# Optimization experiments

Hardware: AMD Instinct MI355X
Metric: run time of the kernel (lower is better)

Reference implementation:

```python
import jax, jax.numpy as jnp
import numpy as np

R, M, A = 512, 256, 256
B, L = 64, 4096


def setup_inputs() -> dict:
    key = jax.random.key(0)
    k1, k2, k3, k4, k5 = jax.random.split(key, 5)
    return {
        "hidden_state": jax.random.normal(k1, (B, R), dtype=jnp.float32),
        "feature_vectors": jax.random.normal(k2, (B, L, M), dtype=jnp.float32),
        "Wa": jax.random.normal(k3, (A, R), dtype=jnp.float32) / np.sqrt(R),
        "Ua": jax.random.normal(k4, (A, M), dtype=jnp.float32) / np.sqrt(M),
        "w": jax.random.normal(k5, (A, 1), dtype=jnp.float32),
        "ba": jnp.zeros((1, A), dtype=jnp.float32),
    }


def reference(hidden_state, feature_vectors, Wa, Ua, w, ba):
    # q: [B, A] broadcast over L; k: [B, L, A]
    q = hidden_state @ Wa.T + ba                      # [B, A]
    k = jnp.einsum("blm,am->bla", feature_vectors, Ua)  # [B, L, A]
    e = jnp.tanh(q[:, None, :] + k) @ w               # [B, L, 1]
    attn = jax.nn.softmax(e, axis=1)                  # softmax over L
    context = jnp.sum(attn * feature_vectors, axis=1)  # [B, M]
    return context
```

## Files before the change

### kernel.cpp

```cpp
#include <hip/hip_runtime.h>
#include <hip/hip_bf16.h>

#define B_  64
#define R_  512
#define M_  256
#define A_  256
#define L_  4096
#define TR_ 256
#define NT2_ (L_ / TR_)

typedef float    f32x4  __attribute__((ext_vector_type(4)));
typedef _Float16 f16x8  __attribute__((ext_vector_type(8)));
typedef _Float16 f16x4  __attribute__((ext_vector_type(4)));

__global__ __launch_bounds__(256) void k_prep(const float* __restrict__ Ua,
                                              _Float16* __restrict__ UaSw) {
  int gid = blockIdx.x * 256 + threadIdx.x;
  int a  = gid >> 6;
  int m0 = (gid & 63) * 4;
  f32x4 v = *(const f32x4*)(Ua + (size_t)a * M_ + m0);
  int t = a >> 4, l16 = a & 15;
  int s = m0 >> 5, quad = (m0 >> 3) & 3, j = m0 & 7;
  size_t idx = ((size_t)((t * 8 + s) * 64 + l16 * 4 + quad)) * 8 + j;
  f16x4 h;
  h[0] = (_Float16)v.x; h[1] = (_Float16)v.y;
  h[2] = (_Float16)v.z; h[3] = (_Float16)v.w;
  *(f16x4*)(UaSw + idx) = h;
}

__global__ __launch_bounds__(256) void k_q(const float* __restrict__ h,
                                           const float* __restrict__ Wa,
                                           const float* __restrict__ ba,
                                           float* __restrict__ q) {
  int b = blockIdx.x;
  int tid = threadIdx.x;
  int wv = tid >> 6, lane = tid & 63;
  const f32x4* hp = (const f32x4*)(h + (size_t)b * R_ + lane * 8);
  f32x4 h0 = hp[0], h1 = hp[1];
#pragma unroll 4
  for (int i = 0; i < 64; ++i) {
    int a = wv * 64 + i;
    const f32x4* wp = (const f32x4*)(Wa + (size_t)a * R_ + lane * 8);
    f32x4 w0 = wp[0], w1 = wp[1];
    f32x4 pr = h0 * w0 + h1 * w1;
    float p = (pr.x + pr.y) + (pr.z + pr.w);
#pragma unroll
    for (int m = 1; m < 64; m <<= 1) p += __shfl_xor(p, m);
    if (lane == 0) q[b * A_ + a] = p + ba[a];
  }
}

__global__ __launch_bounds__(256, 2) void k_main(const float* __restrict__ fv,
                                                 const _Float16* __restrict__ UaSw,
                                                 const float* __restrict__ q,
                                                 const float* __restrict__ w,
                                                 float* __restrict__ blkmax,
                                                 float* __restrict__ blksum,
                                                 float* __restrict__ blkacc) {
  __shared__ __align__(16) _Float16 sA[4][4096];
  __shared__ float sq[A_];
  __shared__ float sw[A_];
  __shared__ float sE[TR_];
  __shared__ float sRed[8];
  __shared__ float sAcc[4][M_];
  int tid = threadIdx.x;
  int b  = blockIdx.x >> 4;
  int l0 = (blockIdx.x & 15) * TR_;
  int wv = tid >> 6, lane = tid & 63;
  int quad = lane >> 4, l16 = lane & 15;

  sq[tid] = q[b * A_ + tid];
  sw[tid] = w[tid];

  int s_w  = lane >> 3;
  int qd_w = (lane >> 1) & 3;
  int jh_w = (lane & 1) * 4;
  _Float16* wbase = &sA[wv][0];

  f16x8 afrag[4][8];
#pragma unroll
  for (int c = 0; c < 4; ++c) {
    const float* rowp = fv + ((size_t)b * L_ + (size_t)(l0 + wv * 64 + c * 16)) * M_ + lane * 4;
#pragma unroll
    for (int i = 0; i < 16; ++i) {
      f32x4 v = *(const f32x4*)(rowp + (size_t)i * M_);
      f16x4 h;
      h[0] = (_Float16)v.x; h[1] = (_Float16)v.y;
      h[2] = (_Float16)v.z; h[3] = (_Float16)v.w;
      *(f16x4*)(wbase + s_w * 512 + (i * 4 + qd_w) * 8 + jh_w) = h;
    }
#pragma unroll
    for (int s = 0; s < 8; ++s)
      afrag[c][s] = *(const f16x8*)(wbase + s * 512 + (l16 * 4 + quad) * 8);
  }
  __syncthreads();

  float eacc[4][4] = {{0,0,0,0},{0,0,0,0},{0,0,0,0},{0,0,0,0}};

#pragma unroll 2
  for (int t = 0; t < 16; ++t) {
    f32x4 acc0 = 0.f, acc1 = 0.f, acc2 = 0.f, acc3 = 0.f;
    const f16x8* bp = (const f16x8*)(UaSw + ((size_t)(t * 8) * 64 + (l16 * 4 + quad)) * 8);
#pragma unroll
    for (int s = 0; s < 8; ++s) {
      f16x8 bf = bp[s * 64];
      acc0 = __builtin_amdgcn_mfma_f32_16x16x32_f16(afrag[0][s], bf, acc0, 0, 0, 0);
      acc1 = __builtin_amdgcn_mfma_f32_16x16x32_f16(afrag[1][s], bf, acc1, 0, 0, 0);
      acc2 = __builtin_amdgcn_mfma_f32_16x16x32_f16(afrag[2][s], bf, acc2, 0, 0, 0);
      acc3 = __builtin_amdgcn_mfma_f32_16x16x32_f16(afrag[3][s], bf, acc3, 0, 0, 0);
    }
    float qc = sq[t * 16 + l16], wc = sw[t * 16 + l16];
#pragma unroll
    for (int i = 0; i < 4; ++i) {
      float x0 = qc + acc0[i];
      eacc[0][i] += (1.0f - 2.0f * __builtin_amdgcn_rcpf(__expf(2.0f * x0) + 1.0f)) * wc;
      float x1 = qc + acc1[i];
      eacc[1][i] += (1.0f - 2.0f * __builtin_amdgcn_rcpf(__expf(2.0f * x1) + 1.0f)) * wc;
      float x2 = qc + acc2[i];
      eacc[2][i] += (1.0f - 2.0f * __builtin_amdgcn_rcpf(__expf(2.0f * x2) + 1.0f)) * wc;
      float x3 = qc + acc3[i];
      eacc[3][i] += (1.0f - 2.0f * __builtin_amdgcn_rcpf(__expf(2.0f * x3) + 1.0f)) * wc;
    }
  }

#pragma unroll
  for (int c = 0; c < 4; ++c)
#pragma unroll
    for (int i = 0; i < 4; ++i) {
      float v = eacc[c][i];
      v += __shfl_xor(v, 1); v += __shfl_xor(v, 2);
      v += __shfl_xor(v, 4); v += __shfl_xor(v, 8);
      if (l16 == 0) sE[wv * 64 + c * 16 + quad * 4 + i] = v;
    }
  __syncthreads();

  float m = sE[tid];
#pragma unroll
  for (int k = 1; k < 64; k <<= 1) m = fmaxf(m, __shfl_xor(m, k));
  if (lane == 0) sRed[wv] = m;
  __syncthreads();
  float mx = fmaxf(fmaxf(sRed[0], sRed[1]), fmaxf(sRed[2], sRed[3]));

  float p[4];
#pragma unroll
  for (int c = 0; c < 4; ++c) p[c] = __expf(sE[wv * 64 + c * 16 + l16] - mx);

  float ps = (quad == 0) ? ((p[0] + p[1]) + (p[2] + p[3])) : 0.f;
#pragma unroll
  for (int k = 1; k < 64; k <<= 1) ps += __shfl_xor(ps, k);
  if (lane == 0) sRed[4 + wv] = ps;

#pragma unroll
  for (int s = 0; s < 8; ++s) {
    float cj[8];
#pragma unroll
    for (int j = 0; j < 8; ++j)
      cj[j] = p[0] * (float)afrag[0][s][j] + p[1] * (float)afrag[1][s][j] +
              p[2] * (float)afrag[2][s][j] + p[3] * (float)afrag[3][s][j];
#pragma unroll
    for (int k = 1; k < 16; k <<= 1) {
#pragma unroll
      for (int j = 0; j < 8; ++j) cj[j] += __shfl_xor(cj[j], k);
    }
    if (l16 == 0) {
#pragma unroll
      for (int j = 0; j < 8; ++j) sAcc[wv][s * 32 + quad * 8 + j] = cj[j];
    }
  }
  __syncthreads();

  float colsum = (sAcc[0][tid] + sAcc[1][tid]) + (sAcc[2][tid] + sAcc[3][tid]);
  blkacc[(size_t)blockIdx.x * M_ + tid] = colsum;
  if (tid == 0) {
    blkmax[blockIdx.x] = mx;
    blksum[blockIdx.x] = (sRed[4] + sRed[5]) + (sRed[6] + sRed[7]);
  }
}

__global__ __launch_bounds__(256) void k_fin(const float* __restrict__ blkmax,
                                             const float* __restrict__ blksum,
                                             const float* __restrict__ blkacc,
                                             float* __restrict__ out) {
  __shared__ float sSc[NT2_];
  int b = blockIdx.x, t = threadIdx.x;
  float M = -1e30f;
#pragma unroll
  for (int i = 0; i < NT2_; ++i) M = fmaxf(M, blkmax[b * NT2_ + i]);
  if (t < NT2_) sSc[t] = __expf(blkmax[b * NT2_ + t] - M);
  __syncthreads();
  float acc = 0.f, S = 0.f;
#pragma unroll 4
  for (int i = 0; i < NT2_; ++i) {
    float sc = sSc[i];
    S += blksum[b * NT2_ + i] * sc;
    acc += blkacc[(size_t)(b * NT2_ + i) * M_ + t] * sc;
  }
  out[b * M_ + t] = acc / S;
}

extern "C" void kernel_launch(void* const* d_in, const int* in_sizes, int n_in,
                              void* d_out, int out_size, void* d_ws, size_t ws_size,
                              hipStream_t stream) {
  const float* h  = (const float*)d_in[0];
  const float* fv = (const float*)d_in[1];
  const float* Wa = (const float*)d_in[2];
  const float* Ua = (const float*)d_in[3];
  const float* w  = (const float*)d_in[4];
  const float* ba = (const float*)d_in[5];
  float* out = (float*)d_out;

  char* ws = (char*)d_ws;
  float*    q      = (float*)(ws);
  _Float16* UaSw   = (_Float16*)(ws + 65536);
  float*    blkmax = (float*)(ws + 196608);
  float*    blksum = (float*)(ws + 200704);
  float*    blkacc = (float*)(ws + 204800);

  k_prep<<<dim3(64), dim3(256), 0, stream>>>(Ua, UaSw);
  k_q<<<dim3(B_), dim3(256), 0, stream>>>(h, Wa, ba, q);
  k_main<<<dim3(B_ * NT2_), dim3(256), 0, stream>>>(fv, UaSw, q, w, blkmax, blksum, blkacc);
  k_fin<<<dim3(B_), dim3(256), 0, stream>>>(blkmax, blksum, blkacc, out);
}
```

Baseline: 466.1 us.

## Halve rows per block, raise occupancy, and software-prefetch Ua fragments

Each block now processes 128 sequence rows instead of 256, which doubles the grid to 2048 blocks and halves the per-thread A-fragment registers. Launch bounds are raised to 4 waves-per-EU. Ua B-fragments are prefetched one step ahead across the t/s loops. The finalize kernel and workspace offsets are resized for 32 partials per batch. The trade is that each Ua fragment load now feeds only two MFMAs instead of four, doubling total Ua traffic, and there are more partials to merge.

```diff
diff --git a/kernel.cpp b/kernel.cpp
--- a/kernel.cpp
+++ b/kernel.cpp
@@ -6,8 +6,8 @@
 #define M_  256
 #define A_  256
 #define L_  4096
-#define TR_ 256
-#define NT2_ (L_ / TR_)
+#define TR_ 128
+#define NT_ (L_ / TR_)
 
 typedef float    f32x4  __attribute__((ext_vector_type(4)));
 typedef _Float16 f16x8  __attribute__((ext_vector_type(8)));
@@ -50,7 +50,7 @@
   }
 }
 
-__global__ __launch_bounds__(256, 2) void k_main(const float* __restrict__ fv,
+__global__ __launch_bounds__(256, 4) void k_main(const float* __restrict__ fv,
                                                  const _Float16* __restrict__ UaSw,
                                                  const float* __restrict__ q,
                                                  const float* __restrict__ w,
@@ -64,8 +64,8 @@
   __shared__ float sRed[8];
   __shared__ float sAcc[4][M_];
   int tid = threadIdx.x;
-  int b  = blockIdx.x >> 4;
-  int l0 = (blockIdx.x & 15) * TR_;
+  int b  = blockIdx.x >> 5;
+  int l0 = (blockIdx.x & 31) * TR_;
   int wv = tid >> 6, lane = tid & 63;
   int quad = lane >> 4, l16 = lane & 15;
 
@@ -77,11 +77,11 @@
   int jh_w = (lane & 1) * 4;
   _Float16* wbase = &sA[wv][0];
 
-  f16x8 afrag[4][8];
-#pragma unroll
-  for (int c = 0; c < 4; ++c) {
-    const float* rowp = fv + ((size_t)b * L_ + (size_t)(l0 + wv * 64 + c * 16)) * M_ + lane * 4;
-#pragma unroll
+  f16x8 afrag[2][8];
+#pragma unroll
+  for (int c = 0; c < 2; ++c) {
+    const float* rowp = fv + ((size_t)b * L_ + (size_t)(l0 + wv * 32 + c * 16)) * M_ + lane * 4;
+#pragma unroll 8
     for (int i = 0; i < 16; ++i) {
       f32x4 v = *(const f32x4*)(rowp + (size_t)i * M_);
       f16x4 h;
@@ -95,57 +95,53 @@
   }
   __syncthreads();
 
-  float eacc[4][4] = {{0,0,0,0},{0,0,0,0},{0,0,0,0},{0,0,0,0}};
-
-#pragma unroll 2
+  float eacc[2][4] = {{0.f, 0.f, 0.f, 0.f}, {0.f, 0.f, 0.f, 0.f}};
+
+  const f16x8* bptr = (const f16x8*)UaSw + (l16 * 4 + quad);
+  f16x8 bnext = bptr[0];
+
   for (int t = 0; t < 16; ++t) {
-    f32x4 acc0 = 0.f, acc1 = 0.f, acc2 = 0.f, acc3 = 0.f;
-    const f16x8* bp = (const f16x8*)(UaSw + ((size_t)(t * 8) * 64 + (l16 * 4 + quad)) * 8);
+    float qc = sq[t * 16 + l16], wc = sw[t * 16 + l16];
+    f32x4 acc0 = 0.f, acc1 = 0.f;
 #pragma unroll
     for (int s = 0; s < 8; ++s) {
-      f16x8 bf = bp[s * 64];
+      f16x8 bf = bnext;
+      int ts = t * 8 + s + 1; if (ts > 127) ts = 127;
+      bnext = bptr[(size_t)ts * 64];
       acc0 = __builtin_amdgcn_mfma_f32_16x16x32_f16(afrag[0][s], bf, acc0, 0, 0, 0);
       acc1 = __builtin_amdgcn_mfma_f32_16x16x32_f16(afrag[1][s], bf, acc1, 0, 0, 0);
-      acc2 = __builtin_amdgcn_mfma_f32_16x16x32_f16(afrag[2][s], bf, acc2, 0, 0, 0);
-      acc3 = __builtin_amdgcn_mfma_f32_16x16x32_f16(afrag[3][s], bf, acc3, 0, 0, 0);
-    }
-    float qc = sq[t * 16 + l16], wc = sw[t * 16 + l16];
+    }
 #pragma unroll
     for (int i = 0; i < 4; ++i) {
       float x0 = qc + acc0[i];
       eacc[0][i] += (1.0f - 2.0f * __builtin_amdgcn_rcpf(__expf(2.0f * x0) + 1.0f)) * wc;
       float x1 = qc + acc1[i];
       eacc[1][i] += (1.0f - 2.0f * __builtin_amdgcn_rcpf(__expf(2.0f * x1) + 1.0f)) * wc;
-      float x2 = qc + acc2[i];
-      eacc[2][i] += (1.0f - 2.0f * __builtin_amdgcn_rcpf(__expf(2.0f * x2) + 1.0f)) * wc;
-      float x3 = qc + acc3[i];
-      eacc[3][i] += (1.0f - 2.0f * __builtin_amdgcn_rcpf(__expf(2.0f * x3) + 1.0f)) * wc;
-    }
-  }
-
-#pragma unroll
-  for (int c = 0; c < 4; ++c)
+    }
+  }
+
+#pragma unroll
+  for (int c = 0; c < 2; ++c)
 #pragma unroll
     for (int i = 0; i < 4; ++i) {
       float v = eacc[c][i];
       v += __shfl_xor(v, 1); v += __shfl_xor(v, 2);
       v += __shfl_xor(v, 4); v += __shfl_xor(v, 8);
-      if (l16 == 0) sE[wv * 64 + c * 16 + quad * 4 + i] = v;
-    }
-  __syncthreads();
-
-  float m = sE[tid];
+      if (l16 == 0) sE[wv * 32 + c * 16 + quad * 4 + i] = v;
+    }
+  __syncthreads();
+
+  float m = (tid < TR_) ? sE[tid] : -1e30f;
 #pragma unroll
   for (int k = 1; k < 64; k <<= 1) m = fmaxf(m, __shfl_xor(m, k));
   if (lane == 0) sRed[wv] = m;
   __syncthreads();
   float mx = fmaxf(fmaxf(sRed[0], sRed[1]), fmaxf(sRed[2], sRed[3]));
 
-  float p[4];
-#pragma unroll
-  for (int c = 0; c < 4; ++c) p[c] = __expf(sE[wv * 64 + c * 16 + l16] - mx);
-
-  float ps = (quad == 0) ? ((p[0] + p[1]) + (p[2] + p[3])) : 0.f;
+  float p0 = __expf(sE[wv * 32 + l16] - mx);
+  float p1 = __expf(sE[wv * 32 + 16 + l16] - mx);
+
+  float ps = (quad == 0) ? (p0 + p1) : 0.f;
 #pragma unroll
   for (int k = 1; k < 64; k <<= 1) ps += __shfl_xor(ps, k);
   if (lane == 0) sRed[4 + wv] = ps;
@@ -155,8 +151,7 @@
     float cj[8];
 #pragma unroll
     for (int j = 0; j < 8; ++j)
-      cj[j] = p[0] * (float)afrag[0][s][j] + p[1] * (float)afrag[1][s][j] +
-              p[2] * (float)afrag[2][s][j] + p[3] * (float)afrag[3][s][j];
+      cj[j] = p0 * (float)afrag[0][s][j] + p1 * (float)afrag[1][s][j];
 #pragma unroll
     for (int k = 1; k < 16; k <<= 1) {
 #pragma unroll
@@ -181,19 +176,19 @@
                                              const float* __restrict__ blksum,
                                              const float* __restrict__ blkacc,
                                              float* __restrict__ out) {
-  __shared__ float sSc[NT2_];
+  __shared__ float sSc[NT_];
   int b = blockIdx.x, t = threadIdx.x;
   float M = -1e30f;
 #pragma unroll
-  for (int i = 0; i < NT2_; ++i) M = fmaxf(M, blkmax[b * NT2_ + i]);
-  if (t < NT2_) sSc[t] = __expf(blkmax[b * NT2_ + t] - M);
+  for (int i = 0; i < NT_; ++i) M = fmaxf(M, blkmax[b * NT_ + i]);
+  if (t < NT_) sSc[t] = __expf(blkmax[b * NT_ + t] - M);
   __syncthreads();
   float acc = 0.f, S = 0.f;
 #pragma unroll 4
-  for (int i = 0; i < NT2_; ++i) {
+  for (int i = 0; i < NT_; ++i) {
     float sc = sSc[i];
-    S += blksum[b * NT2_ + i] * sc;
-    acc += blkacc[(size_t)(b * NT2_ + i) * M_ + t] * sc;
+    S += blksum[b * NT_ + i] * sc;
+    acc += blkacc[(size_t)(b * NT_ + i) * M_ + t] * sc;
   }
   out[b * M_ + t] = acc / S;
 }
@@ -213,11 +208,11 @@
   float*    q      = (float*)(ws);
   _Float16* UaSw   = (_Float16*)(ws + 65536);
   float*    blkmax = (float*)(ws + 196608);
-  float*    blksum = (float*)(ws + 200704);
-  float*    blkacc = (float*)(ws + 204800);
+  float*    blksum = (float*)(ws + 204800);
+  float*    blkacc = (float*)(ws + 212992);
 
   k_prep<<<dim3(64), dim3(256), 0, stream>>>(Ua, UaSw);
   k_q<<<dim3(B_), dim3(256), 0, stream>>>(h, Wa, ba, q);
-  k_main<<<dim3(B_ * NT2_), dim3(256), 0, stream>>>(fv, UaSw, q, w, blkmax, blksum, blkacc);
+  k_main<<<dim3(B_ * NT_), dim3(256), 0, stream>>>(fv, UaSw, q, w, blkmax, blksum, blkacc);
   k_fin<<<dim3(B_), dim3(256), 0, stream>>>(blkmax, blksum, blkacc, out);
 }
```

After: 484.5 us. 3.9% more time.
